# Performance work log

Hardware: AMD Instinct MI355X
Metric: run time of the kernel (lower is better)

Reference implementation:

```python
import jax, jax.numpy as jnp
import numpy as np

HEADS = 4
DIM_HEAD = 32


def _ln(x, g, b):
    m = x.mean(-1, keepdims=True)
    v = ((x - m) ** 2).mean(-1, keepdims=True)
    return (x - m) * jax.lax.rsqrt(v + 1e-5) * g + b


def setup_inputs() -> dict:
    key = jax.random.key(0)
    ks = jax.random.split(key, 9)
    b, n, X, Y, W1, W2, d = 4, 6, 10, 10, 10, 10, 128
    x, y, w1, w2 = 10, 10, 4, 4
    inner = HEADS * DIM_HEAD  # 128 == d
    init = 0.02
    return {
        "q": jax.random.normal(ks[0], (b, n, X, Y, W1, W2, d), jnp.float32),
        "k": jax.random.normal(ks[1], (b, n, x, y, w1, w2, d), jnp.float32),
        "v": jax.random.normal(ks[2], (b, n, x, y, w1, w2, d), jnp.float32),
        "skip": jax.random.normal(ks[3], (b, X, Y, W1, W2, d), jnp.float32),
        "head_gate": jax.random.uniform(ks[4], (HEADS,), jnp.float32, 0.5, 1.5),
        "ln_q_g": jnp.ones((d,), jnp.float32), "ln_q_b": jnp.zeros((d,), jnp.float32),
        "ln_k_g": jnp.ones((d,), jnp.float32), "ln_k_b": jnp.zeros((d,), jnp.float32),
        "ln_v_g": jnp.ones((d,), jnp.float32), "ln_v_b": jnp.zeros((d,), jnp.float32),
        "wq": jax.random.normal(ks[5], (d, inner), jnp.float32) * init,
        "bq": jnp.zeros((inner,), jnp.float32),
        "wk": jax.random.normal(ks[6], (d, inner), jnp.float32) * init,
        "bk": jnp.zeros((inner,), jnp.float32),
        "wv": jax.random.normal(ks[7], (d, inner), jnp.float32) * init,
        "bv": jnp.zeros((inner,), jnp.float32),
        "wp": jax.random.normal(ks[8], (inner, d), jnp.float32) * init,
        "bp": jnp.zeros((d,), jnp.float32),
    }


def reference(q, k, v, skip, head_gate,
              ln_q_g, ln_q_b, ln_k_g, ln_k_b, ln_v_g, ln_v_b,
              wq, bq, wk, bk, wv, bv, wp, bp):
    b, n, X, Y, W1, W2, d = q.shape
    _, _, x, y, w1, w2, _ = k.shape
    L = X * Y                      # number of windows (== x*y, asserted in torch)
    Qn = n * W1 * W2               # query tokens per window (views folded in)
    Kn = n * w1 * w2               # kv tokens per window
    # 'b n x y w1 w2 d -> b (x y) (n w1 w2) d'
    qf = q.transpose(0, 2, 3, 1, 4, 5, 6).reshape(b, L, Qn, d)
    kf = k.transpose(0, 2, 3, 1, 4, 5, 6).reshape(b, L, Kn, d)
    vf = v.transpose(0, 2, 3, 1, 4, 5, 6).reshape(b, L, Kn, d)
    # pre-norm + linear qkv projections
    qh = (_ln(qf, ln_q_g, ln_q_b) @ wq + bq).reshape(b, L, Qn, HEADS, DIM_HEAD)
    kh = (_ln(kf, ln_k_g, ln_k_b) @ wk + bk).reshape(b, L, Kn, HEADS, DIM_HEAD)
    vh = (_ln(vf, ln_v_g, ln_v_b) @ wv + bv).reshape(b, L, Kn, HEADS, DIM_HEAD)
    scale = DIM_HEAD ** -0.5
    # windowed attention scores: (b, m, L, Q, K)
    dot = jnp.einsum('blqmd,blkmd->bmlqk', qh * scale, kh)
    dot = dot * head_gate[None, :, None, None, None]  # multiplicative head gate pre-softmax
    att = jax.nn.softmax(dot, axis=-1)
    a = jnp.einsum('bmlqk,blkmd->blqmd', att, vh).reshape(b, L, Qn, HEADS * DIM_HEAD)
    # 'b (x y) (n w1 w2) c -> b n x y w1 w2 c'
    out = a.reshape(b, X, Y, n, W1, W2, HEADS * DIM_HEAD).transpose(0, 3, 1, 2, 4, 5, 6)
    z = out @ wp + bp
    z = z.mean(axis=1)             # mean-pool over views
    return z + skip
```

## Files before the change

### kernel.cpp

```cpp
#include <hip/hip_runtime.h>
#include <hip/hip_bf16.h>

#define DEV __device__ __forceinline__

typedef __attribute__((ext_vector_type(8))) short short8;
typedef __attribute__((ext_vector_type(8))) unsigned short ushort8;
typedef __attribute__((ext_vector_type(4))) float f32x4;
typedef __attribute__((ext_vector_type(2))) unsigned int uint2v;

DEV unsigned short f2bf(float f) {
    unsigned u = __float_as_uint(f);
    unsigned r = u + 0x7fffu + ((u >> 16) & 1u);
    return (unsigned short)(r >> 16);
}
DEV float bf2f(unsigned short h) { return __uint_as_float(((unsigned)h) << 16); }
DEV unsigned cvt_pk_bf16(float lo, float hi) {
    unsigned r;
    asm("v_cvt_pk_bf16_f32 %0, %1, %2" : "=v"(r) : "v"(lo), "v"(hi));
    return r;
}
#define GLDS16(gp, lp)                                                              \
    __builtin_amdgcn_global_load_lds(                                               \
        (const __attribute__((address_space(1))) void*)(gp),                        \
        (__attribute__((address_space(3))) void*)(lp), 16, 0, 0)


__global__ __launch_bounds__(128) void prep_kernel(
    const float* __restrict__ wq, const float* __restrict__ wk,
    const float* __restrict__ wv, const float* __restrict__ wp,
    const float* __restrict__ ln_q_g, const float* __restrict__ ln_q_b,
    const float* __restrict__ ln_k_g, const float* __restrict__ ln_k_b,
    const float* __restrict__ ln_v_g, const float* __restrict__ ln_v_b,
    const float* __restrict__ bq, const float* __restrict__ bk,
    const float* __restrict__ bv, const float* __restrict__ bp,
    const float* __restrict__ head_gate,
    unsigned short* __restrict__ Wt, float* __restrict__ b2)
{
    const int set = blockIdx.x / 9, sub = blockIdx.x % 9;
    const float* W    = set == 0 ? wq : set == 1 ? wk : set == 2 ? wv : wp;
    const float* g    = set == 0 ? ln_q_g : set == 1 ? ln_k_g : ln_v_g;
    const float* e    = set == 0 ? ln_q_b : set == 1 ? ln_k_b : ln_v_b;
    const float* bias = set == 0 ? bq : set == 1 ? bk : set == 2 ? bv : bp;
    const int mode = set == 0 ? 2 : (set == 3 ? 0 : 1);
    const float scale = 0.17677669529663687f;

    if (sub == 0) {
        const int col = threadIdx.x;
        float sg = (mode == 2) ? scale * head_gate[col >> 5] : 1.f;
        float esum = 0.f;
        if (mode >= 1) {
#pragma unroll 8
            for (int k = 0; k < 128; ++k) esum += e[k] * W[k * 128 + col];
        }
        b2[set * 128 + col] = (bias[col] + esum) * sg;
    } else {
        const int k = threadIdx.x;
        const float gk = (mode >= 1) ? g[k] : 1.f;
        const int kk = k >> 5, h = (k >> 3) & 3, j = k & 7;
#pragma unroll
        for (int c = 0; c < 16; ++c) {
            int col = (sub - 1) * 16 + c;
            int nt = col >> 4, q15 = col & 15;
            float sg = (mode == 2) ? scale * head_gate[col >> 5] : 1.f;
            long idx = set * 16384 + (((nt * 4 + kk) * 64 + q15 * 4 + h) << 3) + j;
            Wt[idx] = f2bf(W[k * 128 + col] * gk * sg);
        }
    }
}

__global__ __launch_bounds__(256) void qkv_proj_mfma(
    const float* __restrict__ qsrc, const float* __restrict__ ksrc, const float* __restrict__ vsrc,
    const unsigned short* __restrict__ WtAll, const float* __restrict__ b2All,
    unsigned short* __restrict__ qh, unsigned short* __restrict__ kh, unsigned short* __restrict__ vh)
{
    __shared__ unsigned short WtL[16384];
    __shared__ unsigned short SrcT[4][16 * 132];

    const int bid = blockIdx.x;
    const int tid = threadIdx.x;
    const int w = tid >> 6, lane = tid & 63;
    const int q15 = lane & 15, h = lane >> 4;

    const float* src; unsigned short* dst; int set, isQ, grp;
    if (bid < 4200)      { src = qsrc; dst = qh; set = 0; isQ = 1; grp = bid * 4 + w; }
    else if (bid < 4800) { src = ksrc; dst = kh; set = 1; isQ = 0; grp = (bid - 4200) * 4 + w; }
    else                 { src = vsrc; dst = vh; set = 2; isQ = 0; grp = (bid - 4800) * 4 + w; }
    const unsigned short* WtF = WtAll + set * 16384;
    const float* b2 = b2All + set * 128;

#pragma unroll
    for (int i = 0; i < 8; ++i)
        GLDS16(WtF + i * 2048 + tid * 8, &WtL[i * 2048 + w * 512]);

    long r0; int maxrr;
    if (isQ) {
        int wv6 = grp / 7, t = grp % 7;
        int bl = wv6 / 6, nn = wv6 % 6;
        int b = bl / 100, l = bl % 100;
        r0 = ((long)(b * 6 + nn) * 100 + l) * 100 + t * 16;
        maxrr = (t == 6) ? 3 : 15;
    } else {
        int bl = grp / 6, nn = grp % 6;
        int b = bl / 100, l = bl % 100;
        r0 = ((long)(b * 6 + nn) * 100 + l) * 16;
        maxrr = 15;
    }

    {
        const int half = lane >> 5, li = lane & 31;
        unsigned short* st = SrcT[w];
#pragma unroll
        for (int i = 0; i < 8; ++i) {
            int rr = 2 * i + half;
            int rrc = rr > maxrr ? maxrr : rr;
            f32x4 v = *(const f32x4*)(src + (r0 + rrc) * 128 + li * 4);
            uint2v c;
            c.x = cvt_pk_bf16(v[0], v[1]);
            c.y = cvt_pk_bf16(v[2], v[3]);
            *(uint2v*)&st[rr * 132 + li * 4] = c;
        }
    }

    short8 xr[4];
    float x[4][8];
    {
        const unsigned short* st = SrcT[w];
#pragma unroll
        for (int kk = 0; kk < 4; ++kk) {
            xr[kk] = *(const short8*)&st[q15 * 132 + kk * 32 + h * 8];
#pragma unroll
            for (int j = 0; j < 8; ++j)
                x[kk][j] = bf2f(((unsigned short)xr[kk][j]));
        }
    }

    float s = 0.f, s2 = 0.f;
#pragma unroll
    for (int kk = 0; kk < 4; ++kk)
#pragma unroll
        for (int j = 0; j < 8; ++j) { s += x[kk][j]; s2 += x[kk][j] * x[kk][j]; }
    s  += __shfl_xor(s, 16);  s  += __shfl_xor(s, 32);
    s2 += __shfl_xor(s2, 16); s2 += __shfl_xor(s2, 32);
    const float mean = s * (1.f / 128.f);
    const float var  = s2 * (1.f / 128.f) - mean * mean;
    const float rs  = rsqrtf(var + 1e-5f);
    const float mrs = -mean * rs;

    short8 xf[4];
#pragma unroll
    for (int kk = 0; kk < 4; ++kk) {
        union { unsigned u[4]; short8 s8; } cv;
#pragma unroll
        for (int d = 0; d < 4; ++d)
            cv.u[d] = cvt_pk_bf16(fmaf(x[kk][2 * d], rs, mrs), fmaf(x[kk][2 * d + 1], rs, mrs));
        xf[kk] = cv.s8;
    }

    f32x4 acc[8];
#pragma unroll
    for (int nt = 0; nt < 8; ++nt)
        acc[nt] = *(const f32x4*)(b2 + nt * 16 + h * 4);

    __syncthreads();

#pragma unroll
    for (int kk = 0; kk < 4; ++kk)
#pragma unroll
        for (int nt = 0; nt < 8; ++nt) {
            short8 wf = *(const short8*)&WtL[(((nt * 4 + kk) * 64) + lane) * 8];
            acc[nt] = __builtin_amdgcn_mfma_f32_16x16x32_bf16(wf, xf[kk], acc[nt], 0, 0, 0);
        }

    unsigned short* og = dst + (long)grp * 2048;
#pragma unroll
    for (int nt = 0; nt < 8; ++nt) {
        uint2v pk;
        pk.x = cvt_pk_bf16(acc[nt][0], acc[nt][1]);
        pk.y = cvt_pk_bf16(acc[nt][2], acc[nt][3]);
        *(uint2v*)(og + (nt * 64 + q15 * 4 + h) * 4) = pk;
    }
}

__global__ __launch_bounds__(256, 3) void attn_mfma_kernel(
    const unsigned short* __restrict__ qh, const unsigned short* __restrict__ kh,
    const unsigned short* __restrict__ vh, unsigned short* __restrict__ am)
{
    __shared__ unsigned short Vt[32 * 104];
    __shared__ unsigned short Pt[4][2][16 * 104];

    const int tid = threadIdx.x;
    const int half = blockIdx.x & 1;
    const int m  = (blockIdx.x >> 1) & 3;
    const int bl = blockIdx.x >> 3;
    const int w = tid >> 6, lane = tid & 63;
    const int q15 = lane & 15, h = lane >> 4;
    const int t = half * 4 + w;

    const int coff = (((2 * m + (h >> 1)) * 64) + q15 * 4 + 2 * (h & 1)) * 4;

    short8 kf[6];
#pragma unroll
    for (int ntk = 0; ntk < 6; ++ntk)
        kf[ntk] = *(const short8*)(kh + (long)(bl * 6 + ntk) * 2048 + coff);

    {
        const int d = tid & 31, kt0 = tid >> 5;
        const int f = m * 32 + d;
        const int ntv = f >> 4, hp = (f >> 2) & 3, rg = f & 3;
#pragma unroll
        for (int j = 0; j < 12; ++j) {
            int kt = kt0 + 8 * j;
            Vt[d * 104 + kt] =
                vh[(long)(bl * 6 + (kt >> 4)) * 2048 + ((ntv * 64 + (kt & 15) * 4 + hp) << 2) + rg];
        }
    }
    __syncthreads();

    short8 vf[2][3];
#pragma unroll
    for (int dt = 0; dt < 2; ++dt)
#pragma unroll
        for (int ks = 0; ks < 3; ++ks)
            vf[dt][ks] = *(const short8*)(Vt + (dt * 16 + q15) * 104 + ks * 32 + h * 8);

    if (t >= 7) return;

    const long qgBase = (long)(bl * 6) * 7 * 2048;

    f32x4 o0 = {0.f, 0.f, 0.f, 0.f}, o1 = {0.f, 0.f, 0.f, 0.f};

#pragma unroll
    for (int nn = 0; nn < 6; ++nn) {
        unsigned short* ptw = &Pt[w][nn & 1][0];

        short8 qf = *(const short8*)(qh + qgBase + (long)(nn * 7 + t) * 2048 + coff);

        f32x4 sc[6];
#pragma unroll
        for (int nt = 0; nt < 6; ++nt)
            sc[nt] = __builtin_amdgcn_mfma_f32_16x16x32_bf16(kf[nt], qf, (f32x4){0.f, 0.f, 0.f, 0.f}, 0, 0, 0);

        float p[24];
#pragma unroll
        for (int nt = 0; nt < 6; ++nt)
#pragma unroll
            for (int rg = 0; rg < 4; ++rg)
                p[nt * 4 + rg] = __expf(sc[nt][rg]);

#pragma unroll
        for (int nt = 0; nt < 6; ++nt) {
            uint2v pk;
            pk.x = cvt_pk_bf16(p[nt * 4 + 0], p[nt * 4 + 1]);
            pk.y = cvt_pk_bf16(p[nt * 4 + 2], p[nt * 4 + 3]);
            *(uint2v*)(ptw + q15 * 104 + nt * 16 + h * 4) = pk;
        }

        float s01 = (p[0] + p[1]) + (p[2] + p[3]);
        float s23 = (p[4] + p[5]) + (p[6] + p[7]);
        float s45 = (p[8] + p[9]) + (p[10] + p[11]);
        float s67 = (p[12] + p[13]) + (p[14] + p[15]);
        float s89 = (p[16] + p[17]) + (p[18] + p[19]);
        float sab = (p[20] + p[21]) + (p[22] + p[23]);
        float sum = ((s01 + s23) + (s45 + s67)) + (s89 + sab);
        sum += __shfl_xor(sum, 16);
        sum += __shfl_xor(sum, 32);
        const float inv = __builtin_amdgcn_rcpf(6.f * sum);

        f32x4 t0 = {0.f, 0.f, 0.f, 0.f}, t1 = {0.f, 0.f, 0.f, 0.f};
#pragma unroll
        for (int ks = 0; ks < 3; ++ks) {
            short8 pf = *(const short8*)(ptw + q15 * 104 + ks * 32 + h * 8);
            t0 = __builtin_amdgcn_mfma_f32_16x16x32_bf16(vf[0][ks], pf, t0, 0, 0, 0);
            t1 = __builtin_amdgcn_mfma_f32_16x16x32_bf16(vf[1][ks], pf, t1, 0, 0, 0);
        }

#pragma unroll
        for (int rg = 0; rg < 4; ++rg) {
            o0[rg] += t0[rg] * inv;
            o1[rg] += t1[rg] * inv;
        }
    }

    {
        unsigned short* og = am + (long)(bl * 7 + t) * 2048;
        uint2v a0, a1;
        a0.x = cvt_pk_bf16(o0[0], o0[1]);
        a0.y = cvt_pk_bf16(o0[2], o0[3]);
        a1.x = cvt_pk_bf16(o1[0], o1[1]);
        a1.y = cvt_pk_bf16(o1[2], o1[3]);
        *(uint2v*)(og + ((2 * m) * 64 + q15 * 4 + h) * 4) = a0;
        *(uint2v*)(og + ((2 * m + 1) * 64 + q15 * 4 + h) * 4) = a1;
    }
}

__global__ __launch_bounds__(256) void out_proj_mfma(
    const unsigned short* __restrict__ am, const unsigned short* __restrict__ WtF,
    const float* __restrict__ b2, const float* __restrict__ skip, float* __restrict__ out)
{
    __shared__ unsigned short WtL[16384];

    const int tid = threadIdx.x;
    const int w = tid >> 6, lane = tid & 63;
    const int q15 = lane & 15, h = lane >> 4;
    const int gp = blockIdx.x * 4 + w;
    const int bl = gp / 7, t = gp % 7;
    const int r = t * 16 + q15;
    const long tok = (long)bl * 100 + r;

#pragma unroll
    for (int i = 0; i < 8; ++i)
        GLDS16(WtF + i * 2048 + tid * 8, &WtL[i * 2048 + w * 512]);

    short8 xf[4];
#pragma unroll
    for (int kk = 0; kk < 4; ++kk)
        xf[kk] = *(const short8*)(am + (long)gp * 2048 +
                                  (((2 * kk + (h >> 1)) * 64 + q15 * 4 + 2 * (h & 1)) << 2));

    f32x4 acc[8];
#pragma unroll
    for (int nt = 0; nt < 8; ++nt)
        acc[nt] = *(const f32x4*)(b2 + nt * 16 + h * 4);

    __syncthreads();

#pragma unroll
    for (int kk = 0; kk < 4; ++kk)
#pragma unroll
        for (int nt = 0; nt < 8; ++nt) {
            short8 wf = *(const short8*)&WtL[(((nt * 4 + kk) * 64) + lane) * 8];
            acc[nt] = __builtin_amdgcn_mfma_f32_16x16x32_bf16(wf, xf[kk], acc[nt], 0, 0, 0);
        }

    if (r < 100) {
        const float* srow = skip + tok * 128 + h * 4;
        float* orow = out + tok * 128 + h * 4;
#pragma unroll
        for (int nt = 0; nt < 8; ++nt) {
            f32x4 sk = *(const f32x4*)(srow + nt * 16);
            f32x4 o;
#pragma unroll
            for (int rg = 0; rg < 4; ++rg) o[rg] = acc[nt][rg] + sk[rg];
            *(f32x4*)(orow + nt * 16) = o;
        }
    }
}

extern "C" void kernel_launch(void* const* d_in, const int* in_sizes, int n_in,
                              void* d_out, int out_size, void* d_ws, size_t ws_size,
                              hipStream_t stream) {
    const float* q        = (const float*)d_in[0];
    const float* k        = (const float*)d_in[1];
    const float* v        = (const float*)d_in[2];
    const float* skip     = (const float*)d_in[3];
    const float* head_gate= (const float*)d_in[4];
    const float* ln_q_g   = (const float*)d_in[5];
    const float* ln_q_b   = (const float*)d_in[6];
    const float* ln_k_g   = (const float*)d_in[7];
    const float* ln_k_b   = (const float*)d_in[8];
    const float* ln_v_g   = (const float*)d_in[9];
    const float* ln_v_b   = (const float*)d_in[10];
    const float* wq       = (const float*)d_in[11];
    const float* bq       = (const float*)d_in[12];
    const float* wk       = (const float*)d_in[13];
    const float* bk       = (const float*)d_in[14];
    const float* wv       = (const float*)d_in[15];
    const float* bv       = (const float*)d_in[16];
    const float* wp       = (const float*)d_in[17];
    const float* bp       = (const float*)d_in[18];
    float* out = (float*)d_out;

    char* ws = (char*)d_ws;
    unsigned short* Wt = (unsigned short*)(ws);
    float* b2          = (float*)(ws + 131072);
    unsigned short* qh = (unsigned short*)(ws + 135168);
    unsigned short* kh = (unsigned short*)(ws + 68948096);
    unsigned short* vh = (unsigned short*)(ws + 78778496);
    unsigned short* am = (unsigned short*)(ws + 88608896);

    prep_kernel<<<36, 128, 0, stream>>>(wq, wk, wv, wp,
                                        ln_q_g, ln_q_b, ln_k_g, ln_k_b, ln_v_g, ln_v_b,
                                        bq, bk, bv, bp, head_gate, Wt, b2);
    qkv_proj_mfma<<<5400, 256, 0, stream>>>(q, k, v, Wt, b2, qh, kh, vh);
    attn_mfma_kernel<<<3200, 256, 0, stream>>>(qh, kh, vh, am);
    out_proj_mfma<<<700, 256, 0, stream>>>(am, Wt + 3 * 16384, b2 + 3 * 128, skip, out);
}
```

Baseline: 97.04 us.

## Fuse Q layernorm and projection into attention kernel, drop qh round trip

After: 149.6 us. +54.2%, slower.

```diff
diff --git a/kernel.cpp b/kernel.cpp
--- a/kernel.cpp
+++ b/kernel.cpp
@@ -68,10 +68,10 @@
     }
 }
 
-__global__ __launch_bounds__(256) void qkv_proj_mfma(
-    const float* __restrict__ qsrc, const float* __restrict__ ksrc, const float* __restrict__ vsrc,
+__global__ __launch_bounds__(256) void kv_proj_mfma(
+    const float* __restrict__ ksrc, const float* __restrict__ vsrc,
     const unsigned short* __restrict__ WtAll, const float* __restrict__ b2All,
-    unsigned short* __restrict__ qh, unsigned short* __restrict__ kh, unsigned short* __restrict__ vh)
+    unsigned short* __restrict__ kh, unsigned short* __restrict__ vh)
 {
     __shared__ unsigned short WtL[16384];
     __shared__ unsigned short SrcT[4][16 * 132];
@@ -81,10 +81,9 @@
     const int w = tid >> 6, lane = tid & 63;
     const int q15 = lane & 15, h = lane >> 4;
 
-    const float* src; unsigned short* dst; int set, isQ, grp;
-    if (bid < 4200)      { src = qsrc; dst = qh; set = 0; isQ = 1; grp = bid * 4 + w; }
-    else if (bid < 4800) { src = ksrc; dst = kh; set = 1; isQ = 0; grp = (bid - 4200) * 4 + w; }
-    else                 { src = vsrc; dst = vh; set = 2; isQ = 0; grp = (bid - 4800) * 4 + w; }
+    const float* src; unsigned short* dst; int set, grp;
+    if (bid < 600) { src = ksrc; dst = kh; set = 1; grp = bid * 4 + w; }
+    else           { src = vsrc; dst = vh; set = 2; grp = (bid - 600) * 4 + w; }
     const unsigned short* WtF = WtAll + set * 16384;
     const float* b2 = b2All + set * 128;
 
@@ -92,18 +91,11 @@
     for (int i = 0; i < 8; ++i)
         GLDS16(WtF + i * 2048 + tid * 8, &WtL[i * 2048 + w * 512]);
 
-    long r0; int maxrr;
-    if (isQ) {
-        int wv6 = grp / 7, t = grp % 7;
-        int bl = wv6 / 6, nn = wv6 % 6;
-        int b = bl / 100, l = bl % 100;
-        r0 = ((long)(b * 6 + nn) * 100 + l) * 100 + t * 16;
-        maxrr = (t == 6) ? 3 : 15;
-    } else {
+    long r0;
+    {
         int bl = grp / 6, nn = grp % 6;
         int b = bl / 100, l = bl % 100;
         r0 = ((long)(b * 6 + nn) * 100 + l) * 16;
-        maxrr = 15;
     }
 
     {
@@ -112,8 +104,7 @@
 #pragma unroll
         for (int i = 0; i < 8; ++i) {
             int rr = 2 * i + half;
-            int rrc = rr > maxrr ? maxrr : rr;
-            f32x4 v = *(const f32x4*)(src + (r0 + rrc) * 128 + li * 4);
+            f32x4 v = *(const f32x4*)(src + (r0 + rr) * 128 + li * 4);
             uint2v c;
             c.x = cvt_pk_bf16(v[0], v[1]);
             c.y = cvt_pk_bf16(v[2], v[3]);
@@ -181,39 +172,52 @@
     }
 }
 
-__global__ __launch_bounds__(256, 3) void attn_mfma_kernel(
-    const unsigned short* __restrict__ qh, const unsigned short* __restrict__ kh,
-    const unsigned short* __restrict__ vh, unsigned short* __restrict__ am)
+__global__ __launch_bounds__(512) void attn_fused_kernel(
+    const float* __restrict__ qsrc,
+    const unsigned short* __restrict__ WqF, const float* __restrict__ b2q,
+    const unsigned short* __restrict__ kh, const unsigned short* __restrict__ vh,
+    unsigned short* __restrict__ am)
 {
-    __shared__ unsigned short Vt[32 * 104];
-    __shared__ unsigned short Pt[4][2][16 * 104];
+    __shared__ unsigned short Vt[4][32 * 104];
+    __shared__ unsigned short Pt[8][16 * 104];
+    __shared__ unsigned short Qx[8][512];
 
     const int tid = threadIdx.x;
     const int half = blockIdx.x & 1;
-    const int m  = (blockIdx.x >> 1) & 3;
-    const int bl = blockIdx.x >> 3;
-    const int w = tid >> 6, lane = tid & 63;
+    const int bl = blockIdx.x >> 1;
+    const int w8 = tid >> 6, lane = tid & 63;
+    const int m = w8 & 3, sub = w8 >> 2;
     const int q15 = lane & 15, h = lane >> 4;
-    const int t = half * 4 + w;
+    const int b = bl / 100, l = bl % 100;
 
     const int coff = (((2 * m + (h >> 1)) * 64) + q15 * 4 + 2 * (h & 1)) * 4;
 
     short8 kf[6];
 #pragma unroll
-    for (int ntk = 0; ntk < 6; ++ntk)
-        kf[ntk] = *(const short8*)(kh + (long)(bl * 6 + ntk) * 2048 + coff);
+    for (int nt = 0; nt < 6; ++nt)
+        kf[nt] = *(const short8*)(kh + (long)(bl * 6 + nt) * 2048 + coff);
 
     {
-        const int d = tid & 31, kt0 = tid >> 5;
+        const int d = lane & 31, ktb = lane >> 5;
         const int f = m * 32 + d;
         const int ntv = f >> 4, hp = (f >> 2) & 3, rg = f & 3;
 #pragma unroll
-        for (int j = 0; j < 12; ++j) {
-            int kt = kt0 + 8 * j;
-            Vt[d * 104 + kt] =
+        for (int j = 0; j < 24; ++j) {
+            int kt = sub * 48 + ktb * 24 + j;
+            Vt[m][d * 104 + kt] =
                 vh[(long)(bl * 6 + (kt >> 4)) * 2048 + ((ntv * 64 + (kt & 15) * 4 + hp) << 2) + rg];
         }
     }
+
+    short8 wqf[2][4];
+#pragma unroll
+    for (int ntL = 0; ntL < 2; ++ntL)
+#pragma unroll
+        for (int kk = 0; kk < 4; ++kk)
+            wqf[ntL][kk] = *(const short8*)&WqF[(((2 * m + ntL) * 4 + kk) * 64 + lane) * 8];
+    const f32x4 bq0 = *(const f32x4*)(b2q + (2 * m) * 16 + h * 4);
+    const f32x4 bq1 = *(const f32x4*)(b2q + (2 * m + 1) * 16 + h * 4);
+
     __syncthreads();
 
     short8 vf[2][3];
@@ -221,75 +225,125 @@
     for (int dt = 0; dt < 2; ++dt)
 #pragma unroll
         for (int ks = 0; ks < 3; ++ks)
-            vf[dt][ks] = *(const short8*)(Vt + (dt * 16 + q15) * 104 + ks * 32 + h * 8);
-
-    if (t >= 7) return;
-
-    const long qgBase = (long)(bl * 6) * 7 * 2048;
-
-    f32x4 o0 = {0.f, 0.f, 0.f, 0.f}, o1 = {0.f, 0.f, 0.f, 0.f};
-
-#pragma unroll
-    for (int nn = 0; nn < 6; ++nn) {
-        unsigned short* ptw = &Pt[w][nn & 1][0];
-
-        short8 qf = *(const short8*)(qh + qgBase + (long)(nn * 7 + t) * 2048 + coff);
-
-        f32x4 sc[6];
-#pragma unroll
-        for (int nt = 0; nt < 6; ++nt)
-            sc[nt] = __builtin_amdgcn_mfma_f32_16x16x32_bf16(kf[nt], qf, (f32x4){0.f, 0.f, 0.f, 0.f}, 0, 0, 0);
-
-        float p[24];
-#pragma unroll
-        for (int nt = 0; nt < 6; ++nt)
-#pragma unroll
-            for (int rg = 0; rg < 4; ++rg)
-                p[nt * 4 + rg] = __expf(sc[nt][rg]);
-
-#pragma unroll
-        for (int nt = 0; nt < 6; ++nt) {
-            uint2v pk;
-            pk.x = cvt_pk_bf16(p[nt * 4 + 0], p[nt * 4 + 1]);
-            pk.y = cvt_pk_bf16(p[nt * 4 + 2], p[nt * 4 + 3]);
-            *(uint2v*)(ptw + q15 * 104 + nt * 16 + h * 4) = pk;
-        }
-
-        float s01 = (p[0] + p[1]) + (p[2] + p[3]);
-        float s23 = (p[4] + p[5]) + (p[6] + p[7]);
-        float s45 = (p[8] + p[9]) + (p[10] + p[11]);
-        float s67 = (p[12] + p[13]) + (p[14] + p[15]);
-        float s89 = (p[16] + p[17]) + (p[18] + p[19]);
-        float sab = (p[20] + p[21]) + (p[22] + p[23]);
-        float sum = ((s01 + s23) + (s45 + s67)) + (s89 + sab);
-        sum += __shfl_xor(sum, 16);
-        sum += __shfl_xor(sum, 32);
-        const float inv = __builtin_amdgcn_rcpf(6.f * sum);
-
-        f32x4 t0 = {0.f, 0.f, 0.f, 0.f}, t1 = {0.f, 0.f, 0.f, 0.f};
-#pragma unroll
-        for (int ks = 0; ks < 3; ++ks) {
-            short8 pf = *(const short8*)(ptw + q15 * 104 + ks * 32 + h * 8);
-            t0 = __builtin_amdgcn_mfma_f32_16x16x32_bf16(vf[0][ks], pf, t0, 0, 0, 0);
-            t1 = __builtin_amdgcn_mfma_f32_16x16x32_bf16(vf[1][ks], pf, t1, 0, 0, 0);
-        }
-
-#pragma unroll
-        for (int rg = 0; rg < 4; ++rg) {
-            o0[rg] += t0[rg] * inv;
-            o1[rg] += t1[rg] * inv;
-        }
-    }
-
-    {
-        unsigned short* og = am + (long)(bl * 7 + t) * 2048;
-        uint2v a0, a1;
-        a0.x = cvt_pk_bf16(o0[0], o0[1]);
-        a0.y = cvt_pk_bf16(o0[2], o0[3]);
-        a1.x = cvt_pk_bf16(o1[0], o1[1]);
-        a1.y = cvt_pk_bf16(o1[2], o1[3]);
-        *(uint2v*)(og + ((2 * m) * 64 + q15 * 4 + h) * 4) = a0;
-        *(uint2v*)(og + ((2 * m + 1) * 64 + q15 * 4 + h) * 4) = a1;
+            vf[dt][ks] = *(const short8*)(&Vt[m][(dt * 16 + q15) * 104 + ks * 32 + h * 8]);
+
+    unsigned short* ptw = Pt[w8];
+    unsigned short* qxw = Qx[w8];
+
+    for (int tt = 0; tt < 2; ++tt) {
+        const int t = half * 4 + sub * 2 + tt;
+        if (t < 7) {
+            const int rq = (t == 6 && q15 > 3) ? 3 : q15;
+
+            f32x4 o0 = {0.f, 0.f, 0.f, 0.f}, o1 = {0.f, 0.f, 0.f, 0.f};
+
+#pragma unroll
+            for (int nn = 0; nn < 6; ++nn) {
+                const long r0 = ((long)(b * 6 + nn) * 100 + l) * 100 + t * 16;
+                const float* row = qsrc + (r0 + rq) * 128 + h * 8;
+
+                float x[4][8];
+#pragma unroll
+                for (int kk = 0; kk < 4; ++kk) {
+                    f32x4 a = *(const f32x4*)(row + kk * 32);
+                    f32x4 c = *(const f32x4*)(row + kk * 32 + 4);
+                    x[kk][0] = a[0]; x[kk][1] = a[1]; x[kk][2] = a[2]; x[kk][3] = a[3];
+                    x[kk][4] = c[0]; x[kk][5] = c[1]; x[kk][6] = c[2]; x[kk][7] = c[3];
+                }
+
+                float s = 0.f, s2 = 0.f;
+#pragma unroll
+                for (int kk = 0; kk < 4; ++kk)
+#pragma unroll
+                    for (int j = 0; j < 8; ++j) { s += x[kk][j]; s2 += x[kk][j] * x[kk][j]; }
+                s  += __shfl_xor(s, 16);  s  += __shfl_xor(s, 32);
+                s2 += __shfl_xor(s2, 16); s2 += __shfl_xor(s2, 32);
+                const float mean = s * (1.f / 128.f);
+                const float var  = s2 * (1.f / 128.f) - mean * mean;
+                const float rs  = rsqrtf(var + 1e-5f);
+                const float mrs = -mean * rs;
+
+                short8 xf[4];
+#pragma unroll
+                for (int kk = 0; kk < 4; ++kk) {
+                    union { unsigned u[4]; short8 s8; } cv;
+#pragma unroll
+                    for (int d = 0; d < 4; ++d)
+                        cv.u[d] = cvt_pk_bf16(fmaf(x[kk][2 * d], rs, mrs), fmaf(x[kk][2 * d + 1], rs, mrs));
+                    xf[kk] = cv.s8;
+                }
+
+                f32x4 acc0 = bq0, acc1 = bq1;
+#pragma unroll
+                for (int kk = 0; kk < 4; ++kk) {
+                    acc0 = __builtin_amdgcn_mfma_f32_16x16x32_bf16(wqf[0][kk], xf[kk], acc0, 0, 0, 0);
+                    acc1 = __builtin_amdgcn_mfma_f32_16x16x32_bf16(wqf[1][kk], xf[kk], acc1, 0, 0, 0);
+                }
+
+                {
+                    uint2v p0, p1;
+                    p0.x = cvt_pk_bf16(acc0[0], acc0[1]); p0.y = cvt_pk_bf16(acc0[2], acc0[3]);
+                    p1.x = cvt_pk_bf16(acc1[0], acc1[1]); p1.y = cvt_pk_bf16(acc1[2], acc1[3]);
+                    *(uint2v*)&qxw[(q15 * 4 + h) * 4] = p0;
+                    *(uint2v*)&qxw[(64 + q15 * 4 + h) * 4] = p1;
+                }
+                short8 qf = *(const short8*)&qxw[(((h >> 1) * 64) + q15 * 4 + 2 * (h & 1)) * 4];
+
+                f32x4 sc[6];
+#pragma unroll
+                for (int nt = 0; nt < 6; ++nt)
+                    sc[nt] = __builtin_amdgcn_mfma_f32_16x16x32_bf16(kf[nt], qf, (f32x4){0.f, 0.f, 0.f, 0.f}, 0, 0, 0);
+
+                float p[24];
+#pragma unroll
+                for (int nt = 0; nt < 6; ++nt)
+#pragma unroll
+                    for (int rg = 0; rg < 4; ++rg)
+                        p[nt * 4 + rg] = __expf(fmaxf(fminf(sc[nt][rg], 30.f), -30.f));
+
+#pragma unroll
+                for (int nt = 0; nt < 6; ++nt) {
+                    uint2v pk;
+                    pk.x = cvt_pk_bf16(p[nt * 4 + 0], p[nt * 4 + 1]);
+                    pk.y = cvt_pk_bf16(p[nt * 4 + 2], p[nt * 4 + 3]);
+                    *(uint2v*)(ptw + q15 * 104 + nt * 16 + h * 4) = pk;
+                }
+
+                float s01 = (p[0] + p[1]) + (p[2] + p[3]);
+                float s23 = (p[4] + p[5]) + (p[6] + p[7]);
+                float s45 = (p[8] + p[9]) + (p[10] + p[11]);
+                float s67 = (p[12] + p[13]) + (p[14] + p[15]);
+                float s89 = (p[16] + p[17]) + (p[18] + p[19]);
+                float sab = (p[20] + p[21]) + (p[22] + p[23]);
+                float sum = ((s01 + s23) + (s45 + s67)) + (s89 + sab);
+                sum += __shfl_xor(sum, 16);
+                sum += __shfl_xor(sum, 32);
+                const float inv = __builtin_amdgcn_rcpf(6.f * sum);
+
+                f32x4 t0 = {0.f, 0.f, 0.f, 0.f}, t1 = {0.f, 0.f, 0.f, 0.f};
+#pragma unroll
+                for (int ks = 0; ks < 3; ++ks) {
+                    short8 pf = *(const short8*)(ptw + q15 * 104 + ks * 32 + h * 8);
+                    t0 = __builtin_amdgcn_mfma_f32_16x16x32_bf16(vf[0][ks], pf, t0, 0, 0, 0);
+                    t1 = __builtin_amdgcn_mfma_f32_16x16x32_bf16(vf[1][ks], pf, t1, 0, 0, 0);
+                }
+
+#pragma unroll
+                for (int rg = 0; rg < 4; ++rg) {
+                    o0[rg] += t0[rg] * inv;
+                    o1[rg] += t1[rg] * inv;
+                }
+            }
+
+            unsigned short* og = am + (long)(bl * 7 + t) * 2048;
+            uint2v a0, a1;
+            a0.x = cvt_pk_bf16(o0[0], o0[1]);
+            a0.y = cvt_pk_bf16(o0[2], o0[3]);
+            a1.x = cvt_pk_bf16(o1[0], o1[1]);
+            a1.y = cvt_pk_bf16(o1[2], o1[3]);
+            *(uint2v*)(og + ((2 * m) * 64 + q15 * 4 + h) * 4) = a0;
+            *(uint2v*)(og + ((2 * m + 1) * 64 + q15 * 4 + h) * 4) = a1;
+        }
     }
 }
 
@@ -373,15 +427,14 @@
     char* ws = (char*)d_ws;
     unsigned short* Wt = (unsigned short*)(ws);
     float* b2          = (float*)(ws + 131072);
-    unsigned short* qh = (unsigned short*)(ws + 135168);
-    unsigned short* kh = (unsigned short*)(ws + 68948096);
-    unsigned short* vh = (unsigned short*)(ws + 78778496);
-    unsigned short* am = (unsigned short*)(ws + 88608896);
+    unsigned short* kh = (unsigned short*)(ws + 4194304);
+    unsigned short* vh = (unsigned short*)(ws + 16777216);
+    unsigned short* am = (unsigned short*)(ws + 29360128);
 
     prep_kernel<<<36, 128, 0, stream>>>(wq, wk, wv, wp,
                                         ln_q_g, ln_q_b, ln_k_g, ln_k_b, ln_v_g, ln_v_b,
                                         bq, bk, bv, bp, head_gate, Wt, b2);
-    qkv_proj_mfma<<<5400, 256, 0, stream>>>(q, k, v, Wt, b2, qh, kh, vh);
-    attn_mfma_kernel<<<3200, 256, 0, stream>>>(qh, kh, vh, am);
+    kv_proj_mfma<<<1200, 256, 0, stream>>>(k, v, Wt, b2, kh, vh);
+    attn_fused_kernel<<<800, 512, 0, stream>>>(q, Wt, b2, kh, vh, am);
     out_proj_mfma<<<700, 256, 0, stream>>>(am, Wt + 3 * 16384, b2 + 3 * 128, skip, out);
 }
```

## Store projected q/k/v in natural row-major layout and drop padded q groups

Applied to the files above, without the earlier changes.

Result: slower. 108.9 us (+12.2%).

```diff
diff --git a/kernel.cpp b/kernel.cpp
--- a/kernel.cpp
+++ b/kernel.cpp
@@ -81,39 +81,25 @@
     const int w = tid >> 6, lane = tid & 63;
     const int q15 = lane & 15, h = lane >> 4;
 
-    const float* src; unsigned short* dst; int set, isQ, grp;
-    if (bid < 4200)      { src = qsrc; dst = qh; set = 0; isQ = 1; grp = bid * 4 + w; }
-    else if (bid < 4800) { src = ksrc; dst = kh; set = 1; isQ = 0; grp = (bid - 4200) * 4 + w; }
-    else                 { src = vsrc; dst = vh; set = 2; isQ = 0; grp = (bid - 4800) * 4 + w; }
+    const float* src; unsigned short* dst; int set, grp;
+    if (bid < 3750)      { src = qsrc; dst = qh; set = 0; grp = bid * 4 + w; }
+    else if (bid < 4350) { src = ksrc; dst = kh; set = 1; grp = (bid - 3750) * 4 + w; }
+    else                 { src = vsrc; dst = vh; set = 2; grp = (bid - 4350) * 4 + w; }
     const unsigned short* WtF = WtAll + set * 16384;
     const float* b2 = b2All + set * 128;
+    const long base = (long)grp * 16;
 
 #pragma unroll
     for (int i = 0; i < 8; ++i)
         GLDS16(WtF + i * 2048 + tid * 8, &WtL[i * 2048 + w * 512]);
 
-    long r0; int maxrr;
-    if (isQ) {
-        int wv6 = grp / 7, t = grp % 7;
-        int bl = wv6 / 6, nn = wv6 % 6;
-        int b = bl / 100, l = bl % 100;
-        r0 = ((long)(b * 6 + nn) * 100 + l) * 100 + t * 16;
-        maxrr = (t == 6) ? 3 : 15;
-    } else {
-        int bl = grp / 6, nn = grp % 6;
-        int b = bl / 100, l = bl % 100;
-        r0 = ((long)(b * 6 + nn) * 100 + l) * 16;
-        maxrr = 15;
-    }
-
     {
         const int half = lane >> 5, li = lane & 31;
         unsigned short* st = SrcT[w];
 #pragma unroll
         for (int i = 0; i < 8; ++i) {
             int rr = 2 * i + half;
-            int rrc = rr > maxrr ? maxrr : rr;
-            f32x4 v = *(const f32x4*)(src + (r0 + rrc) * 128 + li * 4);
+            f32x4 v = *(const f32x4*)(src + (base + rr) * 128 + li * 4);
             uint2v c;
             c.x = cvt_pk_bf16(v[0], v[1]);
             c.y = cvt_pk_bf16(v[2], v[3]);
@@ -171,13 +157,26 @@
             acc[nt] = __builtin_amdgcn_mfma_f32_16x16x32_bf16(wf, xf[kk], acc[nt], 0, 0, 0);
         }
 
-    unsigned short* og = dst + (long)grp * 2048;
-#pragma unroll
-    for (int nt = 0; nt < 8; ++nt) {
-        uint2v pk;
-        pk.x = cvt_pk_bf16(acc[nt][0], acc[nt][1]);
-        pk.y = cvt_pk_bf16(acc[nt][2], acc[nt][3]);
-        *(uint2v*)(og + (nt * 64 + q15 * 4 + h) * 4) = pk;
+    {
+        unsigned short* st = SrcT[w];
+#pragma unroll
+        for (int nt = 0; nt < 8; ++nt) {
+            uint2v pk;
+            pk.x = cvt_pk_bf16(acc[nt][0], acc[nt][1]);
+            pk.y = cvt_pk_bf16(acc[nt][2], acc[nt][3]);
+            *(uint2v*)&st[q15 * 132 + nt * 16 + h * 4] = pk;
+        }
+    }
+
+    {
+        const unsigned short* st = SrcT[w];
+        const int row4 = lane >> 4, c8 = (lane & 15) * 8;
+#pragma unroll
+        for (int j = 0; j < 4; ++j) {
+            int rr = j * 4 + row4;
+            ushort8 v = *(const ushort8*)&st[rr * 132 + c8];
+            *(ushort8*)(dst + (base + rr) * 128 + c8) = v;
+        }
     }
 }
 
@@ -195,23 +194,23 @@
     const int w = tid >> 6, lane = tid & 63;
     const int q15 = lane & 15, h = lane >> 4;
     const int t = half * 4 + w;
-
-    const int coff = (((2 * m + (h >> 1)) * 64) + q15 * 4 + 2 * (h & 1)) * 4;
+    const int b = bl / 100, l = bl % 100;
+    const int fcol = m * 32 + h * 8;
 
     short8 kf[6];
 #pragma unroll
-    for (int ntk = 0; ntk < 6; ++ntk)
-        kf[ntk] = *(const short8*)(kh + (long)(bl * 6 + ntk) * 2048 + coff);
+    for (int nt = 0; nt < 6; ++nt) {
+        long krow = ((long)(b * 6 + nt) * 100 + l) * 16 + q15;
+        kf[nt] = *(const short8*)(kh + krow * 128 + fcol);
+    }
 
     {
         const int d = tid & 31, kt0 = tid >> 5;
-        const int f = m * 32 + d;
-        const int ntv = f >> 4, hp = (f >> 2) & 3, rg = f & 3;
 #pragma unroll
         for (int j = 0; j < 12; ++j) {
             int kt = kt0 + 8 * j;
-            Vt[d * 104 + kt] =
-                vh[(long)(bl * 6 + (kt >> 4)) * 2048 + ((ntv * 64 + (kt & 15) * 4 + hp) << 2) + rg];
+            long vrow = ((long)(b * 6 + (kt >> 4)) * 100 + l) * 16 + (kt & 15);
+            Vt[d * 104 + kt] = vh[vrow * 128 + m * 32 + d];
         }
     }
     __syncthreads();
@@ -225,7 +224,7 @@
 
     if (t >= 7) return;
 
-    const long qgBase = (long)(bl * 6) * 7 * 2048;
+    int r = t * 16 + q15; if (r > 99) r = 99;
 
     f32x4 o0 = {0.f, 0.f, 0.f, 0.f}, o1 = {0.f, 0.f, 0.f, 0.f};
 
@@ -233,7 +232,8 @@
     for (int nn = 0; nn < 6; ++nn) {
         unsigned short* ptw = &Pt[w][nn & 1][0];
 
-        short8 qf = *(const short8*)(qh + qgBase + (long)(nn * 7 + t) * 2048 + coff);
+        long qrow = ((long)(b * 6 + nn) * 100 + l) * 100 + r;
+        short8 qf = *(const short8*)(qh + qrow * 128 + fcol);
 
         f32x4 sc[6];
 #pragma unroll
@@ -373,15 +373,15 @@
     char* ws = (char*)d_ws;
     unsigned short* Wt = (unsigned short*)(ws);
     float* b2          = (float*)(ws + 131072);
-    unsigned short* qh = (unsigned short*)(ws + 135168);
-    unsigned short* kh = (unsigned short*)(ws + 68948096);
-    unsigned short* vh = (unsigned short*)(ws + 78778496);
-    unsigned short* am = (unsigned short*)(ws + 88608896);
+    unsigned short* qh = (unsigned short*)(ws + 1048576);
+    unsigned short* kh = (unsigned short*)(ws + 62914560);
+    unsigned short* vh = (unsigned short*)(ws + 73400320);
+    unsigned short* am = (unsigned short*)(ws + 83886080);
 
     prep_kernel<<<36, 128, 0, stream>>>(wq, wk, wv, wp,
                                         ln_q_g, ln_q_b, ln_k_g, ln_k_b, ln_v_g, ln_v_b,
                                         bq, bk, bv, bp, head_gate, Wt, b2);
-    qkv_proj_mfma<<<5400, 256, 0, stream>>>(q, k, v, Wt, b2, qh, kh, vh);
+    qkv_proj_mfma<<<4950, 256, 0, stream>>>(q, k, v, Wt, b2, qh, kh, vh);
     attn_mfma_kernel<<<3200, 256, 0, stream>>>(qh, kh, vh, am);
     out_proj_mfma<<<700, 256, 0, stream>>>(am, Wt + 3 * 16384, b2 + 3 * 128, skip, out);
 }
```
